# Performance work log

Measured on AMD Instinct MI355X. Metric: run time of the kernel, lower is better.

The kernel has to match this reference:

```python
import jax, jax.numpy as jnp
import numpy as np

EPS = 1e-5
COMMITMENT_COST = 0.25


def setup_inputs() -> dict:
    key = jax.random.key(0)
    k1, k2 = jax.random.split(key)
    inputs = jax.random.normal(k1, (8, 4096, 1024), dtype=jnp.float32)
    ln_weight = jnp.ones((1024,), dtype=jnp.float32)
    ln_bias = jnp.zeros((1024,), dtype=jnp.float32)
    emb = jax.random.normal(k2, (4, 64, 256), dtype=jnp.float32)
    # codebook rows are unit-normalized in __init__
    emb = emb / jnp.maximum(jnp.linalg.norm(emb, axis=-1, keepdims=True), EPS)
    return {"inputs": inputs, "ln_weight": ln_weight, "ln_bias": ln_bias, "embeddings": emb}


def reference(inputs, ln_weight, ln_bias, embeddings):
    # inputs: [B,T,D]; embeddings: [H,K,d] with D = H*d
    B, T, D = inputs.shape
    H, K, d = embeddings.shape

    # LayerNorm (eps=1e-5) + soft clamp tanh(x/5)*5
    mu = jnp.mean(inputs, axis=-1, keepdims=True)
    var = jnp.mean(jnp.square(inputs - mu), axis=-1, keepdims=True)
    x = (inputs - mu) * jax.lax.rsqrt(var + 1e-5) * ln_weight + ln_bias
    x = jnp.tanh(x / 5.0) * 5.0

    # L2-normalize over the FULL embedding dim (matches F.normalize(dim=-1))
    nrm = jnp.linalg.norm(x, axis=-1, keepdims=True)
    xn = x / jnp.maximum(nrm, EPS)

    flat = xn.reshape(-1, H, d)  # [N,H,d]
    # cosine scores against each head's codebook: [N,H,K]
    dist = jnp.einsum("nhd,hkd->nhk", flat, embeddings)
    idx = jnp.argmax(dist, axis=-1)  # [N,H] int

    # per-head gather of codebook vectors
    q = embeddings[jnp.arange(H)[None, :], idx]  # [N,H,d]
    q = q.reshape(B, T, D)

    e_latent_loss = jnp.mean(jnp.square(jax.lax.stop_gradient(q) - xn))
    loss = COMMITMENT_COST * e_latent_loss  # eval mode: entropy_loss = 0

    # straight-through estimator (note: against post-tanh x, not xn)
    quantized = x + jax.lax.stop_gradient(q - x)

    present = jnp.zeros((K,), dtype=bool).at[idx.reshape(-1)].set(True)
    unique_count = jnp.sum(present).astype(jnp.int32)
    return quantized, loss, unique_count
```

## Files before the change

kernel.cpp:

```cpp
#include <hip/hip_runtime.h>
#include <cstdint>
#include <cstddef>

#define NROWS   32768
#define DIM     1024
#define NH      4
#define HD      256
#define NK      64
#define RPB     16
#define NBLK    (NROWS / RPB)
#define THREADS 1024

typedef __attribute__((ext_vector_type(8))) short short8;
typedef __attribute__((ext_vector_type(4))) float float4a;

__device__ __forceinline__ unsigned short f2bf(float f) {
  unsigned int u = __float_as_uint(f);
  u += 0x7fffu + ((u >> 16) & 1u);
  return (unsigned short)(u >> 16);
}
__device__ __forceinline__ float bflo(unsigned int u) {
  return __uint_as_float(u << 16);
}
__device__ __forceinline__ float bfhi(unsigned int u) {
  return __uint_as_float(u & 0xffff0000u);
}

__global__ __launch_bounds__(256) void vq_pre(const float* __restrict__ emb,
                                              unsigned short* __restrict__ ws_emb) {
  const int gid  = blockIdx.x * 256 + threadIdx.x;
  const int lane = gid & 63;
  const int w    = gid >> 6;
  const int s = w & 7, ht = w >> 3, t = ht & 3, h = ht >> 2;
  const int code = t * 16 + (lane & 15);
  const int d0   = s * 32 + (lane >> 4) * 8;
  const float* p = emb + ((size_t)(h * NK + code)) * HD + d0;
  unsigned int w0 = f2bf(p[0]) | ((unsigned int)f2bf(p[1]) << 16);
  unsigned int w1 = f2bf(p[2]) | ((unsigned int)f2bf(p[3]) << 16);
  unsigned int w2 = f2bf(p[4]) | ((unsigned int)f2bf(p[5]) << 16);
  unsigned int w3 = f2bf(p[6]) | ((unsigned int)f2bf(p[7]) << 16);
  uint4 pk = make_uint4(w0, w1, w2, w3);
  *(uint4*)(ws_emb + (size_t)(w * 64 + lane) * 8) = pk;
}

__global__ __launch_bounds__(THREADS, 8) void vq_main(
    const float* __restrict__ in, const float* __restrict__ lnw,
    const float* __restrict__ lnb, const float* __restrict__ emb,
    const unsigned short* __restrict__ ws_emb,
    float* __restrict__ out, float* __restrict__ ws)
{
  __shared__ __align__(16) unsigned short xs[NH * 8 * 4 * 16 * 8];
  __shared__ __align__(16) unsigned short wsh[DIM];
  __shared__ __align__(16) unsigned short bsh[DIM];
  __shared__ float inv_s[RPB];
  __shared__ float base_s[RPB];
  __shared__ __align__(16) int bidx_s[RPB][NH];
  __shared__ float bval_s[RPB][NH];
  __shared__ int flags_s[NH][NK];
  __shared__ float cva[RPB][NH][4];
  __shared__ int   cia[RPB][NH][4];

  float* ws_loss = ws;
  unsigned long long* ws_mask = (unsigned long long*)(ws + NBLK);

  const int tid  = threadIdx.x;
  const int wave = tid >> 6;
  const int lane = tid & 63;
  const int row0 = blockIdx.x * RPB;

  float4 w4, b4;
  if (tid < 256) {
    w4 = *(const float4*)(lnw + tid * 4);
    b4 = *(const float4*)(lnb + tid * 4);
  }

  const int m = wave;
  float4 v[4];
  {
    const float* rp = in + (size_t)(row0 + m) * DIM;
    #pragma unroll
    for (int c = 0; c < 4; ++c) v[c] = *(const float4*)(rp + c * 256 + lane * 4);
  }

  if (tid < 256) {
    flags_s[tid >> 6][tid & 63] = 0;
    uint2 wp, bp;
    wp.x = f2bf(w4.x) | ((unsigned int)f2bf(w4.y) << 16);
    wp.y = f2bf(w4.z) | ((unsigned int)f2bf(w4.w) << 16);
    bp.x = f2bf(b4.x) | ((unsigned int)f2bf(b4.y) << 16);
    bp.y = f2bf(b4.z) | ((unsigned int)f2bf(b4.w) << 16);
    *(uint2*)&wsh[tid * 4] = wp;
    *(uint2*)&bsh[tid * 4] = bp;
  }
  __syncthreads();

  const int sA = lane >> 3;
  const int qA = (lane >> 1) & 3;
  const int hfA = lane & 1;
  const int msw = m ^ (qA << 2) ^ sA;

  float s1 = 0.f, s2 = 0.f;
  #pragma unroll
  for (int c = 0; c < 4; ++c) {
    s1 += (v[c].x + v[c].y) + (v[c].z + v[c].w);
    s2 = fmaf(v[c].x, v[c].x, s2); s2 = fmaf(v[c].y, v[c].y, s2);
    s2 = fmaf(v[c].z, v[c].z, s2); s2 = fmaf(v[c].w, v[c].w, s2);
  }
  #pragma unroll
  for (int d = 1; d < 64; d <<= 1) {
    s1 += __shfl_xor(s1, d, 64);
    s2 += __shfl_xor(s2, d, 64);
  }
  const float mu   = s1 * (1.0f / 1024.0f);
  const float var  = fmaf(-mu, mu, s2 * (1.0f / 1024.0f));
  const float rstd = rsqrtf(var + 1e-5f);

  float ss = 0.f;
  #pragma unroll
  for (int c = 0; c < 4; ++c) {
    const uint2 wu = *(const uint2*)&wsh[c * 256 + lane * 4];
    const uint2 bu = *(const uint2*)&bsh[c * 256 + lane * 4];
    const float wf[4] = { bflo(wu.x), bfhi(wu.x), bflo(wu.y), bfhi(wu.y) };
    const float bf[4] = { bflo(bu.x), bfhi(bu.x), bflo(bu.y), bfhi(bu.y) };
    float* pv = reinterpret_cast<float*>(&v[c]);
    #pragma unroll
    for (int i = 0; i < 4; ++i) {
      float xh = (pv[i] - mu) * rstd;
      xh = fmaf(xh, wf[i], bf[i]);
      const float e = __expf(0.4f * xh);
      const float t = 1.f - 2.f * __builtin_amdgcn_rcpf(e + 1.f);
      const float xx = 5.f * t;
      ss = fmaf(xx, xx, ss);
      pv[i] = xx;
    }
    const int gran = ((c * 8 + sA) * 4 + qA) * 16 + msw;
    uint2 pk;
    pk.x = f2bf(v[c].x) | ((unsigned int)f2bf(v[c].y) << 16);
    pk.y = f2bf(v[c].z) | ((unsigned int)f2bf(v[c].w) << 16);
    *(uint2*)&xs[gran * 8 + hfA * 4] = pk;
  }
  #pragma unroll
  for (int d = 1; d < 64; d <<= 1) ss += __shfl_xor(ss, d, 64);

  if (lane == 0) {
    const float nrm = sqrtf(ss);
    const float iv  = 1.f / fmaxf(nrm, 1e-5f);
    inv_s[m]  = iv;
    base_s[m] = fmaf(ss * iv, iv, 4.f);
  }
  __syncthreads();

  {
    const int h = wave >> 2, t = wave & 3;
    const int q = lane >> 4, mm = lane & 15;

    short8 afr[8];
    #pragma unroll
    for (int s = 0; s < 8; ++s) {
      const int gran = (h * 8 + s) * 64 + q * 16 + (mm ^ (q << 2) ^ s);
      afr[s] = *(const short8*)&xs[gran * 8];
    }

    const short8* eb = (const short8*)ws_emb + (size_t)h * 2048 + lane;
    float4a acc;
    #pragma unroll
    for (int r = 0; r < 4; ++r) acc[r] = 0.f;
    #pragma unroll
    for (int s = 0; s < 8; ++s) {
      const short8 bfr = eb[(t * 8 + s) * 64];
      acc = __builtin_amdgcn_mfma_f32_16x16x32_bf16(afr[s], bfr, acc, 0, 0, 0);
    }

    #pragma unroll
    for (int r = 0; r < 4; ++r) {
      float bv = acc[r];
      int   bi = t * 16 + mm;
      #pragma unroll
      for (int d = 1; d <= 8; d <<= 1) {
        const float ov = __shfl_xor(bv, d, 64);
        const int   oi = __shfl_xor(bi, d, 64);
        if (ov > bv || (ov == bv && oi < bi)) { bv = ov; bi = oi; }
      }
      if (mm == 0) {
        const int row = q * 4 + r;
        cva[row][h][t] = bv;
        cia[row][h][t] = bi;
      }
    }
  }
  __syncthreads();

  if (tid < 64) {
    const int row = tid >> 2, h = tid & 3;
    float wv = cva[row][h][0];
    int   win = cia[row][h][0];
    #pragma unroll
    for (int t = 1; t < 4; ++t) {
      const float v1 = cva[row][h][t];
      const int   i1 = cia[row][h][t];
      if (v1 > wv) { wv = v1; win = i1; }
    }
    bidx_s[row][h] = win;
    bval_s[row][h] = wv;
    flags_s[h][win] = 1;
  }
  __syncthreads();

  {
    const int row = wave;
    const int4 bi = *(const int4*)(&bidx_s[row][0]);
    const float4 q0 = *(const float4*)(emb + (size_t)(0 * NK + bi.x) * HD + lane * 4);
    const float4 q1 = *(const float4*)(emb + (size_t)(1 * NK + bi.y) * HD + lane * 4);
    const float4 q2 = *(const float4*)(emb + (size_t)(2 * NK + bi.z) * HD + lane * 4);
    const float4 q3 = *(const float4*)(emb + (size_t)(3 * NK + bi.w) * HD + lane * 4);
    float* op = out + (size_t)(row0 + row) * DIM + lane * 4;
    *(float4*)(op + 0)   = q0;
    *(float4*)(op + 256) = q1;
    *(float4*)(op + 512) = q2;
    *(float4*)(op + 768) = q3;
  }

  if (wave == 0) {
    float lsum = 0.f;
    if (lane < RPB) {
      const float ds = (bval_s[lane][0] + bval_s[lane][1]) +
                       (bval_s[lane][2] + bval_s[lane][3]);
      lsum = fmaf(-2.f * inv_s[lane], ds, base_s[lane]);
    }
    #pragma unroll
    for (int d = 1; d <= 8; d <<= 1) lsum += __shfl_xor(lsum, d, 64);
    if (lane == 0) ws_loss[blockIdx.x] = lsum;
  } else if (wave == 1) {
    const int f = flags_s[0][lane] | flags_s[1][lane] |
                  flags_s[2][lane] | flags_s[3][lane];
    const unsigned long long mk = __ballot(f != 0);
    if (lane == 0) ws_mask[blockIdx.x] = mk;
  }
}

__global__ __launch_bounds__(256) void vq_fin(const float* __restrict__ ws,
                                              float* __restrict__ out) {
  __shared__ float ls[4];
  __shared__ unsigned long long ms[4];
  const float* ws_loss = ws;
  const unsigned long long* ws_mask = (const unsigned long long*)(ws + NBLK);

  const int tid = threadIdx.x, wave = tid >> 6, lane = tid & 63;
  float l = 0.f;
  unsigned long long m = 0ull;
  for (int i = tid; i < NBLK; i += 256) { l += ws_loss[i]; m |= ws_mask[i]; }
  #pragma unroll
  for (int s = 1; s < 64; s <<= 1) {
    l += __shfl_xor(l, s, 64);
    m |= __shfl_xor(m, s, 64);
  }
  if (lane == 0) { ls[wave] = l; ms[wave] = m; }
  __syncthreads();
  if (tid == 0) {
    const float total = (ls[0] + ls[1]) + (ls[2] + ls[3]);
    const unsigned long long mm = ms[0] | ms[1] | ms[2] | ms[3];
    out[33554432] = 0.25f * total / 33554432.0f;
    out[33554433] = (float)__popcll(mm);
  }
}

extern "C" void kernel_launch(void* const* d_in, const int* in_sizes, int n_in,
                              void* d_out, int out_size, void* d_ws, size_t ws_size,
                              hipStream_t stream) {
  const float* in  = (const float*)d_in[0];
  const float* lnw = (const float*)d_in[1];
  const float* lnb = (const float*)d_in[2];
  const float* emb = (const float*)d_in[3];
  float* out = (float*)d_out;
  float* ws  = (float*)d_ws;

  unsigned short* ws_emb = (unsigned short*)((char*)d_ws + 24576);

  vq_pre<<<32, 256, 0, stream>>>(emb, ws_emb);
  vq_main<<<NBLK, THREADS, 0, stream>>>(in, lnw, lnb, emb, ws_emb, out, ws);
  vq_fin<<<1, 256, 0, stream>>>(ws, out);
}
```

Before: 259.2 us.

## Process four row tiles per block with register prefetch of next tile

Result: slower. 289.6 us (+11.7%).

```diff
diff --git a/kernel.cpp b/kernel.cpp
--- a/kernel.cpp
+++ b/kernel.cpp
@@ -1,4 +1,5 @@
 #include <hip/hip_runtime.h>
+#include <hip/hip_bf16.h>
 #include <cstdint>
 #include <cstddef>
 
@@ -8,22 +9,32 @@
 #define HD      256
 #define NK      64
 #define RPB     16
-#define NBLK    (NROWS / RPB)
+#define TPB     4
+#define PBLK    (NROWS / (RPB * TPB))
 #define THREADS 1024
 
 typedef __attribute__((ext_vector_type(8))) short short8;
 typedef __attribute__((ext_vector_type(4))) float float4a;
+typedef __attribute__((ext_vector_type(4))) float f32x4;
 
 __device__ __forceinline__ unsigned short f2bf(float f) {
   unsigned int u = __float_as_uint(f);
   u += 0x7fffu + ((u >> 16) & 1u);
   return (unsigned short)(u >> 16);
 }
+__device__ __forceinline__ unsigned int pk2bf(float a, float b) {
+  __hip_bfloat162 h = __float22bfloat162_rn(make_float2(a, b));
+  return *reinterpret_cast<unsigned int*>(&h);
+}
 __device__ __forceinline__ float bflo(unsigned int u) {
   return __uint_as_float(u << 16);
 }
 __device__ __forceinline__ float bfhi(unsigned int u) {
   return __uint_as_float(u & 0xffff0000u);
+}
+__device__ __forceinline__ void ntst(float* p, float4 v) {
+  __builtin_nontemporal_store(*reinterpret_cast<f32x4*>(&v),
+                              reinterpret_cast<f32x4*>(p));
 }
 
 __global__ __launch_bounds__(256) void vq_pre(const float* __restrict__ emb,
@@ -56,41 +67,35 @@
   __shared__ float base_s[RPB];
   __shared__ __align__(16) int bidx_s[RPB][NH];
   __shared__ float bval_s[RPB][NH];
-  __shared__ int flags_s[NH][NK];
   __shared__ float cva[RPB][NH][4];
   __shared__ int   cia[RPB][NH][4];
+  __shared__ unsigned long long ms4[NH];
 
   float* ws_loss = ws;
-  unsigned long long* ws_mask = (unsigned long long*)(ws + NBLK);
+  unsigned long long* ws_mask = (unsigned long long*)(ws + PBLK);
 
   const int tid  = threadIdx.x;
   const int wave = tid >> 6;
   const int lane = tid & 63;
-  const int row0 = blockIdx.x * RPB;
-
-  float4 w4, b4;
+  const int m    = wave;
+
   if (tid < 256) {
-    w4 = *(const float4*)(lnw + tid * 4);
-    b4 = *(const float4*)(lnb + tid * 4);
-  }
-
-  const int m = wave;
-  float4 v[4];
-  {
-    const float* rp = in + (size_t)(row0 + m) * DIM;
-    #pragma unroll
-    for (int c = 0; c < 4; ++c) v[c] = *(const float4*)(rp + c * 256 + lane * 4);
-  }
-
-  if (tid < 256) {
-    flags_s[tid >> 6][tid & 63] = 0;
+    float4 w4 = *(const float4*)(lnw + tid * 4);
+    float4 b4 = *(const float4*)(lnb + tid * 4);
     uint2 wp, bp;
-    wp.x = f2bf(w4.x) | ((unsigned int)f2bf(w4.y) << 16);
-    wp.y = f2bf(w4.z) | ((unsigned int)f2bf(w4.w) << 16);
-    bp.x = f2bf(b4.x) | ((unsigned int)f2bf(b4.y) << 16);
-    bp.y = f2bf(b4.z) | ((unsigned int)f2bf(b4.w) << 16);
+    wp.x = pk2bf(w4.x, w4.y); wp.y = pk2bf(w4.z, w4.w);
+    bp.x = pk2bf(b4.x, b4.y); bp.y = pk2bf(b4.z, b4.w);
     *(uint2*)&wsh[tid * 4] = wp;
     *(uint2*)&bsh[tid * 4] = bp;
+  }
+
+  const size_t row_base = (size_t)blockIdx.x * (RPB * TPB) + m;
+
+  float4 vn[4];
+  {
+    const float* rp = in + row_base * DIM;
+    #pragma unroll
+    for (int c = 0; c < 4; ++c) vn[c] = *(const float4*)(rp + c * 256 + lane * 4);
   }
   __syncthreads();
 
@@ -99,143 +104,152 @@
   const int hfA = lane & 1;
   const int msw = m ^ (qA << 2) ^ sA;
 
-  float s1 = 0.f, s2 = 0.f;
-  #pragma unroll
-  for (int c = 0; c < 4; ++c) {
-    s1 += (v[c].x + v[c].y) + (v[c].z + v[c].w);
-    s2 = fmaf(v[c].x, v[c].x, s2); s2 = fmaf(v[c].y, v[c].y, s2);
-    s2 = fmaf(v[c].z, v[c].z, s2); s2 = fmaf(v[c].w, v[c].w, s2);
-  }
-  #pragma unroll
-  for (int d = 1; d < 64; d <<= 1) {
-    s1 += __shfl_xor(s1, d, 64);
-    s2 += __shfl_xor(s2, d, 64);
-  }
-  const float mu   = s1 * (1.0f / 1024.0f);
-  const float var  = fmaf(-mu, mu, s2 * (1.0f / 1024.0f));
-  const float rstd = rsqrtf(var + 1e-5f);
-
-  float ss = 0.f;
-  #pragma unroll
-  for (int c = 0; c < 4; ++c) {
-    const uint2 wu = *(const uint2*)&wsh[c * 256 + lane * 4];
-    const uint2 bu = *(const uint2*)&bsh[c * 256 + lane * 4];
-    const float wf[4] = { bflo(wu.x), bfhi(wu.x), bflo(wu.y), bfhi(wu.y) };
-    const float bf[4] = { bflo(bu.x), bfhi(bu.x), bflo(bu.y), bfhi(bu.y) };
-    float* pv = reinterpret_cast<float*>(&v[c]);
-    #pragma unroll
-    for (int i = 0; i < 4; ++i) {
-      float xh = (pv[i] - mu) * rstd;
-      xh = fmaf(xh, wf[i], bf[i]);
-      const float e = __expf(0.4f * xh);
-      const float t = 1.f - 2.f * __builtin_amdgcn_rcpf(e + 1.f);
-      const float xx = 5.f * t;
-      ss = fmaf(xx, xx, ss);
-      pv[i] = xx;
-    }
-    const int gran = ((c * 8 + sA) * 4 + qA) * 16 + msw;
-    uint2 pk;
-    pk.x = f2bf(v[c].x) | ((unsigned int)f2bf(v[c].y) << 16);
-    pk.y = f2bf(v[c].z) | ((unsigned int)f2bf(v[c].w) << 16);
-    *(uint2*)&xs[gran * 8 + hfA * 4] = pk;
-  }
-  #pragma unroll
-  for (int d = 1; d < 64; d <<= 1) ss += __shfl_xor(ss, d, 64);
-
-  if (lane == 0) {
-    const float nrm = sqrtf(ss);
-    const float iv  = 1.f / fmaxf(nrm, 1e-5f);
-    inv_s[m]  = iv;
-    base_s[m] = fmaf(ss * iv, iv, 4.f);
-  }
-  __syncthreads();
-
-  {
-    const int h = wave >> 2, t = wave & 3;
-    const int q = lane >> 4, mm = lane & 15;
-
-    short8 afr[8];
-    #pragma unroll
-    for (int s = 0; s < 8; ++s) {
-      const int gran = (h * 8 + s) * 64 + q * 16 + (mm ^ (q << 2) ^ s);
-      afr[s] = *(const short8*)&xs[gran * 8];
-    }
-
-    const short8* eb = (const short8*)ws_emb + (size_t)h * 2048 + lane;
-    float4a acc;
-    #pragma unroll
-    for (int r = 0; r < 4; ++r) acc[r] = 0.f;
-    #pragma unroll
-    for (int s = 0; s < 8; ++s) {
-      const short8 bfr = eb[(t * 8 + s) * 64];
-      acc = __builtin_amdgcn_mfma_f32_16x16x32_bf16(afr[s], bfr, acc, 0, 0, 0);
-    }
-
-    #pragma unroll
-    for (int r = 0; r < 4; ++r) {
-      float bv = acc[r];
-      int   bi = t * 16 + mm;
-      #pragma unroll
-      for (int d = 1; d <= 8; d <<= 1) {
-        const float ov = __shfl_xor(bv, d, 64);
-        const int   oi = __shfl_xor(bi, d, 64);
-        if (ov > bv || (ov == bv && oi < bi)) { bv = ov; bi = oi; }
-      }
-      if (mm == 0) {
-        const int row = q * 4 + r;
-        cva[row][h][t] = bv;
-        cia[row][h][t] = bi;
-      }
-    }
-  }
-  __syncthreads();
-
-  if (tid < 64) {
-    const int row = tid >> 2, h = tid & 3;
-    float wv = cva[row][h][0];
-    int   win = cia[row][h][0];
-    #pragma unroll
-    for (int t = 1; t < 4; ++t) {
-      const float v1 = cva[row][h][t];
-      const int   i1 = cia[row][h][t];
-      if (v1 > wv) { wv = v1; win = i1; }
-    }
-    bidx_s[row][h] = win;
-    bval_s[row][h] = wv;
-    flags_s[h][win] = 1;
-  }
-  __syncthreads();
-
-  {
-    const int row = wave;
-    const int4 bi = *(const int4*)(&bidx_s[row][0]);
-    const float4 q0 = *(const float4*)(emb + (size_t)(0 * NK + bi.x) * HD + lane * 4);
-    const float4 q1 = *(const float4*)(emb + (size_t)(1 * NK + bi.y) * HD + lane * 4);
-    const float4 q2 = *(const float4*)(emb + (size_t)(2 * NK + bi.z) * HD + lane * 4);
-    const float4 q3 = *(const float4*)(emb + (size_t)(3 * NK + bi.w) * HD + lane * 4);
-    float* op = out + (size_t)(row0 + row) * DIM + lane * 4;
-    *(float4*)(op + 0)   = q0;
-    *(float4*)(op + 256) = q1;
-    *(float4*)(op + 512) = q2;
-    *(float4*)(op + 768) = q3;
-  }
-
-  if (wave == 0) {
-    float lsum = 0.f;
-    if (lane < RPB) {
+  float lacc = 0.f;
+  unsigned long long pres = 0ull;
+
+  for (int t = 0; t < TPB; ++t) {
+    float s1 = 0.f, s2 = 0.f;
+    #pragma unroll
+    for (int c = 0; c < 4; ++c) {
+      s1 += (vn[c].x + vn[c].y) + (vn[c].z + vn[c].w);
+      s2 = fmaf(vn[c].x, vn[c].x, s2); s2 = fmaf(vn[c].y, vn[c].y, s2);
+      s2 = fmaf(vn[c].z, vn[c].z, s2); s2 = fmaf(vn[c].w, vn[c].w, s2);
+    }
+    #pragma unroll
+    for (int d = 1; d < 64; d <<= 1) {
+      s1 += __shfl_xor(s1, d, 64);
+      s2 += __shfl_xor(s2, d, 64);
+    }
+    const float mu   = s1 * (1.0f / 1024.0f);
+    const float var  = fmaf(-mu, mu, s2 * (1.0f / 1024.0f));
+    const float rstd = rsqrtf(var + 1e-5f);
+    const float nmu  = -mu * rstd;
+
+    const float* nrp = in + (row_base + (size_t)(t + 1) * RPB) * DIM;
+
+    float ss = 0.f;
+    #pragma unroll
+    for (int c = 0; c < 4; ++c) {
+      const uint2 wu = *(const uint2*)&wsh[c * 256 + lane * 4];
+      const uint2 bu = *(const uint2*)&bsh[c * 256 + lane * 4];
+      const float wf[4] = { bflo(wu.x), bfhi(wu.x), bflo(wu.y), bfhi(wu.y) };
+      const float bf[4] = { bflo(bu.x), bfhi(bu.x), bflo(bu.y), bfhi(bu.y) };
+      const float4 vv = vn[c];
+      const float pv[4] = { vv.x, vv.y, vv.z, vv.w };
+      float xx[4];
+      #pragma unroll
+      for (int i = 0; i < 4; ++i) {
+        float xh = fmaf(pv[i], rstd, nmu);
+        xh = fmaf(xh, wf[i], bf[i]);
+        const float e = exp2f(xh * 0.57707801635f);
+        const float r = __builtin_amdgcn_rcpf(e + 1.f);
+        const float x = fmaf(-10.f, r, 5.f);
+        ss = fmaf(x, x, ss);
+        xx[i] = x;
+      }
+      const int gran = ((c * 8 + sA) * 4 + qA) * 16 + msw;
+      uint2 pk;
+      pk.x = pk2bf(xx[0], xx[1]);
+      pk.y = pk2bf(xx[2], xx[3]);
+      *(uint2*)&xs[gran * 8 + hfA * 4] = pk;
+      if (t + 1 < TPB) vn[c] = *(const float4*)(nrp + c * 256 + lane * 4);
+    }
+    #pragma unroll
+    for (int d = 1; d < 64; d <<= 1) ss += __shfl_xor(ss, d, 64);
+
+    if (lane == 0) {
+      const float nrm = sqrtf(ss);
+      const float iv  = 1.f / fmaxf(nrm, 1e-5f);
+      inv_s[m]  = iv;
+      base_s[m] = fmaf(ss * iv, iv, 4.f);
+    }
+    __syncthreads();
+
+    {
+      const int h = wave >> 2, tt = wave & 3;
+      const int q = lane >> 4, mm = lane & 15;
+      const short8* eb = (const short8*)ws_emb + (size_t)h * 2048 + lane;
+
+      float4a acc;
+      #pragma unroll
+      for (int r = 0; r < 4; ++r) acc[r] = 0.f;
+      #pragma unroll
+      for (int s = 0; s < 8; ++s) {
+        const int gran = (h * 8 + s) * 64 + q * 16 + (mm ^ (q << 2) ^ s);
+        const short8 a = *(const short8*)&xs[gran * 8];
+        const short8 b = eb[(tt * 8 + s) * 64];
+        acc = __builtin_amdgcn_mfma_f32_16x16x32_bf16(a, b, acc, 0, 0, 0);
+      }
+
+      #pragma unroll
+      for (int r = 0; r < 4; ++r) {
+        float bv = acc[r];
+        int   bi = tt * 16 + mm;
+        #pragma unroll
+        for (int d = 1; d <= 8; d <<= 1) {
+          const float ov = __shfl_xor(bv, d, 64);
+          const int   oi = __shfl_xor(bi, d, 64);
+          if (ov > bv || (ov == bv && oi < bi)) { bv = ov; bi = oi; }
+        }
+        if (mm == 0) {
+          const int row = q * 4 + r;
+          cva[row][h][tt] = bv;
+          cia[row][h][tt] = bi;
+        }
+      }
+    }
+    __syncthreads();
+
+    if (tid < 64) {
+      const int row = tid >> 2, h = tid & 3;
+      float wv = cva[row][h][0];
+      int   win = cia[row][h][0];
+      #pragma unroll
+      for (int k = 1; k < 4; ++k) {
+        const float v1 = cva[row][h][k];
+        const int   i1 = cia[row][h][k];
+        if (v1 > wv) { wv = v1; win = i1; }
+      }
+      bidx_s[row][h] = win;
+      bval_s[row][h] = wv;
+    }
+    __syncthreads();
+
+    {
+      const int4 bi = *(const int4*)(&bidx_s[m][0]);
+      const float4 q0 = *(const float4*)(emb + (size_t)(0 * NK + bi.x) * HD + lane * 4);
+      const float4 q1 = *(const float4*)(emb + (size_t)(1 * NK + bi.y) * HD + lane * 4);
+      const float4 q2 = *(const float4*)(emb + (size_t)(2 * NK + bi.z) * HD + lane * 4);
+      const float4 q3 = *(const float4*)(emb + (size_t)(3 * NK + bi.w) * HD + lane * 4);
+      float* op = out + (row_base + (size_t)t * RPB) * DIM + lane * 4;
+      ntst(op + 0,   q0);
+      ntst(op + 256, q1);
+      ntst(op + 512, q2);
+      ntst(op + 768, q3);
+    }
+
+    if (wave == 0 && lane < RPB) {
       const float ds = (bval_s[lane][0] + bval_s[lane][1]) +
                        (bval_s[lane][2] + bval_s[lane][3]);
-      lsum = fmaf(-2.f * inv_s[lane], ds, base_s[lane]);
-    }
-    #pragma unroll
-    for (int d = 1; d <= 8; d <<= 1) lsum += __shfl_xor(lsum, d, 64);
-    if (lane == 0) ws_loss[blockIdx.x] = lsum;
-  } else if (wave == 1) {
-    const int f = flags_s[0][lane] | flags_s[1][lane] |
-                  flags_s[2][lane] | flags_s[3][lane];
-    const unsigned long long mk = __ballot(f != 0);
-    if (lane == 0) ws_mask[blockIdx.x] = mk;
-  }
+      lacc += fmaf(-2.f * inv_s[lane], ds, base_s[lane]);
+    }
+    if (wave < 4) {
+      int f = 0;
+      #pragma unroll
+      for (int r = 0; r < RPB; ++r) f |= (bidx_s[r][wave] == lane) ? 1 : 0;
+      pres |= __ballot(f != 0);
+    }
+    __syncthreads();
+  }
+
+  if (wave == 0) {
+    #pragma unroll
+    for (int d = 1; d <= 8; d <<= 1) lacc += __shfl_xor(lacc, d, 64);
+    if (lane == 0) ws_loss[blockIdx.x] = lacc;
+  }
+  if (wave < 4 && lane == 0) ms4[wave] = pres;
+  __syncthreads();
+  if (tid == 0) ws_mask[blockIdx.x] = ms4[0] | ms4[1] | ms4[2] | ms4[3];
 }
 
 __global__ __launch_bounds__(256) void vq_fin(const float* __restrict__ ws,
@@ -243,12 +257,12 @@
   __shared__ float ls[4];
   __shared__ unsigned long long ms[4];
   const float* ws_loss = ws;
-  const unsigned long long* ws_mask = (const unsigned long long*)(ws + NBLK);
+  const unsigned long long* ws_mask = (const unsigned long long*)(ws + PBLK);
 
   const int tid = threadIdx.x, wave = tid >> 6, lane = tid & 63;
   float l = 0.f;
   unsigned long long m = 0ull;
-  for (int i = tid; i < NBLK; i += 256) { l += ws_loss[i]; m |= ws_mask[i]; }
+  for (int i = tid; i < PBLK; i += 256) { l += ws_loss[i]; m |= ws_mask[i]; }
   #pragma unroll
   for (int s = 1; s < 64; s <<= 1) {
     l += __shfl_xor(l, s, 64);
@@ -277,6 +291,6 @@
   unsigned short* ws_emb = (unsigned short*)((char*)d_ws + 24576);
 
   vq_pre<<<32, 256, 0, stream>>>(emb, ws_emb);
-  vq_main<<<NBLK, THREADS, 0, stream>>>(in, lnw, lnb, emb, ws_emb, out, ws);
+  vq_main<<<PBLK, THREADS, 0, stream>>>(in, lnw, lnb, emb, ws_emb, out, ws);
   vq_fin<<<1, 256, 0, stream>>>(ws, out);
 }
```

## Use DPP wave reductions, fold per-row argmax into each wave, trim barriers

Applied to the files above, without the earlier changes.

Measured after the change: 249.6 us. -3.7%, faster.

```diff
diff --git a/kernel.cpp b/kernel.cpp
--- a/kernel.cpp
+++ b/kernel.cpp
@@ -1,4 +1,5 @@
 #include <hip/hip_runtime.h>
+#include <hip/hip_bf16.h>
 #include <cstdint>
 #include <cstddef>
 
@@ -19,11 +20,47 @@
   u += 0x7fffu + ((u >> 16) & 1u);
   return (unsigned short)(u >> 16);
 }
+__device__ __forceinline__ unsigned int pk2bf(float a, float b) {
+  __hip_bfloat162 h = __float22bfloat162_rn(make_float2(a, b));
+  return *reinterpret_cast<unsigned int*>(&h);
+}
 __device__ __forceinline__ float bflo(unsigned int u) {
   return __uint_as_float(u << 16);
 }
 __device__ __forceinline__ float bfhi(unsigned int u) {
   return __uint_as_float(u & 0xffff0000u);
+}
+
+template <int CTRL, int RM>
+__device__ __forceinline__ float dpp_add0(float x) {
+  int t = __builtin_amdgcn_update_dpp(0, __float_as_int(x), CTRL, RM, 0xf, true);
+  return x + __int_as_float(t);
+}
+__device__ __forceinline__ float wave_sum(float x) {
+  x = dpp_add0<0x111, 0xf>(x);
+  x = dpp_add0<0x112, 0xf>(x);
+  x = dpp_add0<0x114, 0xf>(x);
+  x = dpp_add0<0x118, 0xf>(x);
+  x = dpp_add0<0x142, 0xa>(x);
+  x = dpp_add0<0x143, 0xc>(x);
+  return __int_as_float(__builtin_amdgcn_readlane(__float_as_int(x), 63));
+}
+template <int CTRL>
+__device__ __forceinline__ void dpp_argmax_step(float& bv, int& bi) {
+  const float ov = __int_as_float(__builtin_amdgcn_update_dpp(
+      __float_as_int(bv), __float_as_int(bv), CTRL, 0xf, 0xf, false));
+  const int oi = __builtin_amdgcn_update_dpp(bi, bi, CTRL, 0xf, 0xf, false);
+  if (ov > bv || (ov == bv && oi < bi)) { bv = ov; bi = oi; }
+}
+__device__ __forceinline__ void row16_argmax(float& bv, int& bi) {
+  dpp_argmax_step<0x111>(bv, bi);
+  dpp_argmax_step<0x112>(bv, bi);
+  dpp_argmax_step<0x114>(bv, bi);
+  dpp_argmax_step<0x118>(bv, bi);
+}
+__device__ __forceinline__ void quad4_argmax(float& bv, int& bi) {
+  dpp_argmax_step<0xB1>(bv, bi);
+  dpp_argmax_step<0x4E>(bv, bi);
 }
 
 __global__ __launch_bounds__(256) void vq_pre(const float* __restrict__ emb,
@@ -52,13 +89,10 @@
   __shared__ __align__(16) unsigned short xs[NH * 8 * 4 * 16 * 8];
   __shared__ __align__(16) unsigned short wsh[DIM];
   __shared__ __align__(16) unsigned short bsh[DIM];
-  __shared__ float inv_s[RPB];
-  __shared__ float base_s[RPB];
-  __shared__ __align__(16) int bidx_s[RPB][NH];
-  __shared__ float bval_s[RPB][NH];
   __shared__ int flags_s[NH][NK];
   __shared__ float cva[RPB][NH][4];
   __shared__ int   cia[RPB][NH][4];
+  __shared__ float rl_s[RPB];
 
   float* ws_loss = ws;
   unsigned long long* ws_mask = (unsigned long long*)(ws + NBLK);
@@ -67,6 +101,7 @@
   const int wave = tid >> 6;
   const int lane = tid & 63;
   const int row0 = blockIdx.x * RPB;
+  const int m    = wave;
 
   float4 w4, b4;
   if (tid < 256) {
@@ -74,7 +109,6 @@
     b4 = *(const float4*)(lnb + tid * 4);
   }
 
-  const int m = wave;
   float4 v[4];
   {
     const float* rp = in + (size_t)(row0 + m) * DIM;
@@ -85,10 +119,8 @@
   if (tid < 256) {
     flags_s[tid >> 6][tid & 63] = 0;
     uint2 wp, bp;
-    wp.x = f2bf(w4.x) | ((unsigned int)f2bf(w4.y) << 16);
-    wp.y = f2bf(w4.z) | ((unsigned int)f2bf(w4.w) << 16);
-    bp.x = f2bf(b4.x) | ((unsigned int)f2bf(b4.y) << 16);
-    bp.y = f2bf(b4.z) | ((unsigned int)f2bf(b4.w) << 16);
+    wp.x = pk2bf(w4.x, w4.y); wp.y = pk2bf(w4.z, w4.w);
+    bp.x = pk2bf(b4.x, b4.y); bp.y = pk2bf(b4.z, b4.w);
     *(uint2*)&wsh[tid * 4] = wp;
     *(uint2*)&bsh[tid * 4] = bp;
   }
@@ -106,14 +138,12 @@
     s2 = fmaf(v[c].x, v[c].x, s2); s2 = fmaf(v[c].y, v[c].y, s2);
     s2 = fmaf(v[c].z, v[c].z, s2); s2 = fmaf(v[c].w, v[c].w, s2);
   }
-  #pragma unroll
-  for (int d = 1; d < 64; d <<= 1) {
-    s1 += __shfl_xor(s1, d, 64);
-    s2 += __shfl_xor(s2, d, 64);
-  }
+  s1 = wave_sum(s1);
+  s2 = wave_sum(s2);
   const float mu   = s1 * (1.0f / 1024.0f);
   const float var  = fmaf(-mu, mu, s2 * (1.0f / 1024.0f));
   const float rstd = rsqrtf(var + 1e-5f);
+  const float nmu  = -mu * rstd;
 
   float ss = 0.f;
   #pragma unroll
@@ -123,113 +153,95 @@
     const float wf[4] = { bflo(wu.x), bfhi(wu.x), bflo(wu.y), bfhi(wu.y) };
     const float bf[4] = { bflo(bu.x), bfhi(bu.x), bflo(bu.y), bfhi(bu.y) };
     float* pv = reinterpret_cast<float*>(&v[c]);
+    float xx[4];
     #pragma unroll
     for (int i = 0; i < 4; ++i) {
-      float xh = (pv[i] - mu) * rstd;
+      float xh = fmaf(pv[i], rstd, nmu);
       xh = fmaf(xh, wf[i], bf[i]);
-      const float e = __expf(0.4f * xh);
-      const float t = 1.f - 2.f * __builtin_amdgcn_rcpf(e + 1.f);
-      const float xx = 5.f * t;
-      ss = fmaf(xx, xx, ss);
-      pv[i] = xx;
+      const float e = exp2f(xh * 0.57707801636f);
+      const float r = __builtin_amdgcn_rcpf(e + 1.f);
+      const float x = fmaf(-10.f, r, 5.f);
+      ss = fmaf(x, x, ss);
+      xx[i] = x;
     }
     const int gran = ((c * 8 + sA) * 4 + qA) * 16 + msw;
     uint2 pk;
-    pk.x = f2bf(v[c].x) | ((unsigned int)f2bf(v[c].y) << 16);
-    pk.y = f2bf(v[c].z) | ((unsigned int)f2bf(v[c].w) << 16);
+    pk.x = pk2bf(xx[0], xx[1]);
+    pk.y = pk2bf(xx[2], xx[3]);
     *(uint2*)&xs[gran * 8 + hfA * 4] = pk;
   }
-  #pragma unroll
-  for (int d = 1; d < 64; d <<= 1) ss += __shfl_xor(ss, d, 64);
-
-  if (lane == 0) {
-    const float nrm = sqrtf(ss);
-    const float iv  = 1.f / fmaxf(nrm, 1e-5f);
-    inv_s[m]  = iv;
-    base_s[m] = fmaf(ss * iv, iv, 4.f);
-  }
+  ss = wave_sum(ss);
+
+  const float nrm  = sqrtf(ss);
+  const float iv   = 1.f / fmaxf(nrm, 1e-5f);
+  const float base = fmaf(ss * iv, iv, 4.f);
   __syncthreads();
 
   {
-    const int h = wave >> 2, t = wave & 3;
+    const int h = wave >> 2, tt = wave & 3;
     const int q = lane >> 4, mm = lane & 15;
-
-    short8 afr[8];
+    const short8* eb = (const short8*)ws_emb + (size_t)h * 2048 + lane;
+
+    float4a acc;
+    #pragma unroll
+    for (int r = 0; r < 4; ++r) acc[r] = 0.f;
     #pragma unroll
     for (int s = 0; s < 8; ++s) {
       const int gran = (h * 8 + s) * 64 + q * 16 + (mm ^ (q << 2) ^ s);
-      afr[s] = *(const short8*)&xs[gran * 8];
-    }
-
-    const short8* eb = (const short8*)ws_emb + (size_t)h * 2048 + lane;
-    float4a acc;
-    #pragma unroll
-    for (int r = 0; r < 4; ++r) acc[r] = 0.f;
-    #pragma unroll
-    for (int s = 0; s < 8; ++s) {
-      const short8 bfr = eb[(t * 8 + s) * 64];
-      acc = __builtin_amdgcn_mfma_f32_16x16x32_bf16(afr[s], bfr, acc, 0, 0, 0);
+      const short8 a = *(const short8*)&xs[gran * 8];
+      const short8 b = eb[(tt * 8 + s) * 64];
+      acc = __builtin_amdgcn_mfma_f32_16x16x32_bf16(a, b, acc, 0, 0, 0);
     }
 
     #pragma unroll
     for (int r = 0; r < 4; ++r) {
       float bv = acc[r];
-      int   bi = t * 16 + mm;
-      #pragma unroll
-      for (int d = 1; d <= 8; d <<= 1) {
-        const float ov = __shfl_xor(bv, d, 64);
-        const int   oi = __shfl_xor(bi, d, 64);
-        if (ov > bv || (ov == bv && oi < bi)) { bv = ov; bi = oi; }
-      }
-      if (mm == 0) {
+      int   bi = tt * 16 + mm;
+      row16_argmax(bv, bi);
+      if (mm == 15) {
         const int row = q * 4 + r;
-        cva[row][h][t] = bv;
-        cia[row][h][t] = bi;
+        cva[row][h][tt] = bv;
+        cia[row][h][tt] = bi;
       }
     }
   }
   __syncthreads();
 
-  if (tid < 64) {
-    const int row = tid >> 2, h = tid & 3;
-    float wv = cva[row][h][0];
-    int   win = cia[row][h][0];
-    #pragma unroll
-    for (int t = 1; t < 4; ++t) {
-      const float v1 = cva[row][h][t];
-      const int   i1 = cia[row][h][t];
-      if (v1 > wv) { wv = v1; win = i1; }
-    }
-    bidx_s[row][h] = win;
-    bval_s[row][h] = wv;
-    flags_s[h][win] = 1;
-  }
-  __syncthreads();
-
   {
-    const int row = wave;
-    const int4 bi = *(const int4*)(&bidx_s[row][0]);
-    const float4 q0 = *(const float4*)(emb + (size_t)(0 * NK + bi.x) * HD + lane * 4);
-    const float4 q1 = *(const float4*)(emb + (size_t)(1 * NK + bi.y) * HD + lane * 4);
-    const float4 q2 = *(const float4*)(emb + (size_t)(2 * NK + bi.z) * HD + lane * 4);
-    const float4 q3 = *(const float4*)(emb + (size_t)(3 * NK + bi.w) * HD + lane * 4);
-    float* op = out + (size_t)(row0 + row) * DIM + lane * 4;
+    const int j = lane & 15;
+    float bv = cva[m][j >> 2][j & 3];
+    int   bi = cia[m][j >> 2][j & 3];
+    quad4_argmax(bv, bi);
+
+    const int b0 = __builtin_amdgcn_readlane(bi, 0);
+    const int b1 = __builtin_amdgcn_readlane(bi, 4);
+    const int b2 = __builtin_amdgcn_readlane(bi, 8);
+    const int b3 = __builtin_amdgcn_readlane(bi, 12);
+
+    const float4 q0 = *(const float4*)(emb + (size_t)(0 * NK + b0) * HD + lane * 4);
+    const float4 q1 = *(const float4*)(emb + (size_t)(1 * NK + b1) * HD + lane * 4);
+    const float4 q2 = *(const float4*)(emb + (size_t)(2 * NK + b2) * HD + lane * 4);
+    const float4 q3 = *(const float4*)(emb + (size_t)(3 * NK + b3) * HD + lane * 4);
+    float* op = out + (size_t)(row0 + m) * DIM + lane * 4;
     *(float4*)(op + 0)   = q0;
     *(float4*)(op + 256) = q1;
     *(float4*)(op + 512) = q2;
     *(float4*)(op + 768) = q3;
-  }
+
+    const float v0 = __int_as_float(__builtin_amdgcn_readlane(__float_as_int(bv), 0));
+    const float v1 = __int_as_float(__builtin_amdgcn_readlane(__float_as_int(bv), 4));
+    const float v2 = __int_as_float(__builtin_amdgcn_readlane(__float_as_int(bv), 8));
+    const float v3 = __int_as_float(__builtin_amdgcn_readlane(__float_as_int(bv), 12));
+    const float ds = (v0 + v1) + (v2 + v3);
+    if (lane == 0) rl_s[m] = fmaf(-2.f * iv, ds, base);
+    if (lane < 16 && (lane & 3) == 0) flags_s[lane >> 2][bi] = 1;
+  }
+  __syncthreads();
 
   if (wave == 0) {
-    float lsum = 0.f;
-    if (lane < RPB) {
-      const float ds = (bval_s[lane][0] + bval_s[lane][1]) +
-                       (bval_s[lane][2] + bval_s[lane][3]);
-      lsum = fmaf(-2.f * inv_s[lane], ds, base_s[lane]);
-    }
-    #pragma unroll
-    for (int d = 1; d <= 8; d <<= 1) lsum += __shfl_xor(lsum, d, 64);
-    if (lane == 0) ws_loss[blockIdx.x] = lsum;
+    float l = (lane < RPB) ? rl_s[lane] : 0.f;
+    l = wave_sum(l);
+    if (lane == 0) ws_loss[blockIdx.x] = l;
   } else if (wave == 1) {
     const int f = flags_s[0][lane] | flags_s[1][lane] |
                   flags_s[2][lane] | flags_s[3][lane];
```
